# Kernel optimization log

Measured on AMD Instinct MI355X. Metric: run time of the kernel, lower is better.

The kernel has to match this reference:

```python
import jax, jax.numpy as jnp
import numpy as np

GROUPS = 32
EPS = 1e-5
NUM_HEADS = 8

def group_norm(x, w, b):
    # x: [B, C, H, W], normalize over (C//G, H, W) per group
    B, C, H, W = x.shape
    xg = x.reshape(B, GROUPS, C // GROUPS, H, W)
    mean = xg.mean(axis=(2, 3, 4), keepdims=True)
    var = xg.var(axis=(2, 3, 4), keepdims=True)
    xg = (xg - mean) * jax.lax.rsqrt(var + EPS)
    x = xg.reshape(B, C, H, W)
    return x * w[None, :, None, None] + b[None, :, None, None]

def setup_inputs() -> dict:
    key = jax.random.key(0)
    ks = jax.random.split(key, 3)
    C = 512
    x = jax.random.normal(ks[0], (8, C, 32, 32), dtype=jnp.float32)
    gn_w = jnp.ones((C,), jnp.float32)
    gn_b = jnp.zeros((C,), jnp.float32)
    # 1x1 conv weights stored as [out, in] matrices
    qkv_w = jax.random.normal(ks[1], (3 * C, C), dtype=jnp.float32) * (C ** -0.5)
    qkv_b = jnp.zeros((3 * C,), jnp.float32)
    proj_w = jax.random.normal(ks[2], (C, C), dtype=jnp.float32) * (C ** -0.5)
    proj_b = jnp.zeros((C,), jnp.float32)
    return {"x": x, "gn_w": gn_w, "gn_b": gn_b, "qkv_w": qkv_w,
            "qkv_b": qkv_b, "proj_w": proj_w, "proj_b": proj_b}

def reference(x, gn_w, gn_b, qkv_w, qkv_b, proj_w, proj_b):
    B, C, H, W = x.shape
    nh = NUM_HEADS
    hd = C // nh
    N = H * W
    residual = x
    xn = group_norm(x, gn_w, gn_b)
    # 1x1 conv == channel matmul: [B, 3C, H, W]
    qkv = jnp.einsum('bchw,oc->bohw', xn, qkv_w) + qkv_b[None, :, None, None]
    # [B, 3, nh, hd, N] -> q/k/v each [B, nh, N, hd]
    qkv = qkv.reshape(B, 3, nh, hd, N).transpose(1, 0, 2, 4, 3)
    q, k, v = qkv[0], qkv[1], qkv[2]
    scale = hd ** -0.5
    attn = jnp.einsum('bhqd,bhkd->bhqk', q, k) * scale
    attn = jax.nn.softmax(attn, axis=-1)
    out = jnp.einsum('bhqk,bhkd->bhqd', attn, v)  # [B, nh, N, hd]
    out = out.transpose(0, 1, 3, 2).reshape(B, C, H, W)
    out = jnp.einsum('bchw,oc->bohw', out, proj_w) + proj_b[None, :, None, None]
    return out + residual
```

## Files before the change

kernel.cpp:

```cpp
#include <hip/hip_runtime.h>


typedef __bf16 bf16;
typedef __bf16 bf16x8 __attribute__((ext_vector_type(8)));
typedef __bf16 bf16x4 __attribute__((ext_vector_type(4)));
typedef float  f32x4  __attribute__((ext_vector_type(4)));

#define MFMA_16x16x32(A, B, C) __builtin_amdgcn_mfma_f32_16x16x32_bf16((A), (B), (C), 0, 0, 0)

static __device__ __forceinline__ void async_stage_128x32(
    const bf16* __restrict__ g0, bf16* lds, int tid) {
  const int wv = tid >> 6, ln = tid & 63;
#pragma unroll
  for (int cc = 0; cc < 2; ++cc) {
    const int c = wv + cc * 4;
    const bf16* g = g0 + (size_t)(c * 16 + (ln >> 2)) * 512 + (ln & 3) * 8;
    __builtin_amdgcn_global_load_lds(
        (const __attribute__((address_space(1))) void*)g,
        (__attribute__((address_space(3))) void*)(lds + c * 512),
        16, 0, 0);
  }
}

static __device__ __forceinline__ void async_stage_64x32(
    const bf16* __restrict__ g0, bf16* lds, int tid) {
  const int wv = tid >> 6, ln = tid & 63;
  const bf16* g = g0 + (size_t)(wv * 16 + (ln >> 2)) * 512 + (ln & 3) * 8;
  __builtin_amdgcn_global_load_lds(
      (const __attribute__((address_space(1))) void*)g,
      (__attribute__((address_space(3))) void*)(lds + wv * 512),
      16, 0, 0);
}

__global__ __launch_bounds__(256) void gn_fused_kernel(
    const float* __restrict__ x,
    const float* __restrict__ gn_w, const float* __restrict__ gn_b,
    const float* __restrict__ qw, const float* __restrict__ pw,
    bf16* __restrict__ wq, bf16* __restrict__ wp, bf16* __restrict__ xn_t) {
  const int t = threadIdx.x;
  if (blockIdx.x >= 256) {
    const int idx = (blockIdx.x - 256) * 256 + t;
    if (idx < 196608) {
      float4 v = ((const float4*)qw)[idx];
      bf16x4 o = { (bf16)v.x, (bf16)v.y, (bf16)v.z, (bf16)v.w };
      *(bf16x4*)(&wq[idx * 4]) = o;
    }
    if (idx < 65536) {
      float4 v = ((const float4*)pw)[idx];
      bf16x4 o = { (bf16)v.x, (bf16)v.y, (bf16)v.z, (bf16)v.w };
      *(bf16x4*)(&wp[idx * 4]) = o;
    }
    return;
  }
  const int bg = blockIdx.x;
  const int b = bg >> 5, g = bg & 31;
  const int c0 = g * 16;
  const float4* p = (const float4*)(x + ((size_t)b * 512 + c0) * 1024);
  float4 v[16];
  float s = 0.f, s2 = 0.f;
#pragma unroll
  for (int i = 0; i < 16; ++i) {
    v[i] = p[t + 256 * i];
    s  += (v[i].x + v[i].y) + (v[i].z + v[i].w);
    s2 += (v[i].x * v[i].x + v[i].y * v[i].y) + (v[i].z * v[i].z + v[i].w * v[i].w);
  }
#pragma unroll
  for (int d = 1; d < 64; d <<= 1) {
    s  += __shfl_xor(s,  d);
    s2 += __shfl_xor(s2, d);
  }
  __shared__ float as[4], as2[4];
  __shared__ float scs[16], shs[16];
  if ((t & 63) == 0) { as[t >> 6] = s; as2[t >> 6] = s2; }
  __syncthreads();
  if (t < 16) {
    float S  = as[0] + as[1] + as[2] + as[3];
    float S2 = as2[0] + as2[1] + as2[2] + as2[3];
    float m  = S * (1.0f / 16384.0f);
    float rs = rsqrtf(S2 * (1.0f / 16384.0f) - m * m + 1e-5f);
    float sc = rs * gn_w[c0 + t];
    scs[t] = sc;
    shs[t] = gn_b[c0 + t] - m * sc;
  }
  __syncthreads();
  bf16* ob = xn_t + ((size_t)b * 1024 + 4 * t) * 512 + c0;
#pragma unroll
  for (int j = 0; j < 4; ++j) {
    bf16 tmp[16];
#pragma unroll
    for (int i = 0; i < 16; ++i) {
      float val = (j == 0) ? v[i].x : (j == 1) ? v[i].y : (j == 2) ? v[i].z : v[i].w;
      tmp[i] = (bf16)(val * scs[i] + shs[i]);
    }
    *(bf16x8*)(ob + (size_t)j * 512)     = *(bf16x8*)(tmp);
    *(bf16x8*)(ob + (size_t)j * 512 + 8) = *(bf16x8*)(tmp + 8);
  }
}

__global__ __launch_bounds__(256) void qkv_gemm_kernel(
    const bf16* __restrict__ W, const bf16* __restrict__ xn_t,
    const float* __restrict__ qkv_b, bf16* __restrict__ qkv_t,
    bf16* __restrict__ v_t) {
  const int n0 = blockIdx.x * 128;
  const int o0 = blockIdx.y * 128;
  const int b  = blockIdx.z;
  __shared__ bf16 As[2][128 * 32];
  __shared__ bf16 Bs[2][128 * 32];
  const int tid = threadIdx.x, ln = tid & 63, wv = tid >> 6;
  const int mw = (wv >> 1) * 64, nw = (wv & 1) * 64;
  const int l15 = ln & 15, lg = ln >> 4;
  const bool isV = (o0 >= 1024);
  const bf16* gA = W + (size_t)o0 * 512;
  const bf16* gB = xn_t + ((size_t)b * 1024 + n0) * 512;
  f32x4 acc[4][4] = {};
  async_stage_128x32(gA, As[0], tid);
  async_stage_128x32(gB, Bs[0], tid);
  for (int it = 0; it < 16; ++it) {
    __syncthreads();
    const int cur = it & 1, nxt = cur ^ 1;
    if (it < 15) {
      async_stage_128x32(gA + (it + 1) * 32, As[nxt], tid);
      async_stage_128x32(gB + (it + 1) * 32, Bs[nxt], tid);
    }
    bf16x8 af[4], bfr[4];
#pragma unroll
    for (int mi = 0; mi < 4; ++mi)
      af[mi] = *(const bf16x8*)(&As[cur][(mw + mi * 16 + l15) * 32 + lg * 8]);
#pragma unroll
    for (int nj = 0; nj < 4; ++nj)
      bfr[nj] = *(const bf16x8*)(&Bs[cur][(nw + nj * 16 + l15) * 32 + lg * 8]);
    if (!isV) {
#pragma unroll
      for (int mi = 0; mi < 4; ++mi)
#pragma unroll
        for (int nj = 0; nj < 4; ++nj)
          acc[mi][nj] = MFMA_16x16x32(af[mi], bfr[nj], acc[mi][nj]);
    } else {
#pragma unroll
      for (int mi = 0; mi < 4; ++mi)
#pragma unroll
        for (int nj = 0; nj < 4; ++nj)
          acc[mi][nj] = MFMA_16x16x32(bfr[nj], af[mi], acc[mi][nj]);
    }
  }
  if (!isV) {
    const float qs = (o0 < 512) ? 0.125f * 1.44269504089f : 1.0f;
#pragma unroll
    for (int mi = 0; mi < 4; ++mi) {
      const int o = o0 + mw + mi * 16 + lg * 4;
      const float b0 = qkv_b[o], b1 = qkv_b[o + 1], b2 = qkv_b[o + 2], b3 = qkv_b[o + 3];
#pragma unroll
      for (int nj = 0; nj < 4; ++nj) {
        const int n = n0 + nw + nj * 16 + l15;
        f32x4 v = acc[mi][nj];
        bf16x4 st = { (bf16)((v.x + b0) * qs), (bf16)((v.y + b1) * qs),
                      (bf16)((v.z + b2) * qs), (bf16)((v.w + b3) * qs) };
        *(bf16x4*)(&qkv_t[((size_t)b * 1024 + n) * 1536 + o]) = st;
      }
    }
  } else {
#pragma unroll
    for (int mi = 0; mi < 4; ++mi) {
      const int o  = o0 + mw + mi * 16 + l15;
      const int hd = o - 1024;
      const float bias = qkv_b[o];
#pragma unroll
      for (int nj = 0; nj < 4; ++nj) {
        const int n = n0 + nw + nj * 16 + lg * 4;
        f32x4 v = acc[mi][nj];
        bf16x4 st = { (bf16)(v.x + bias), (bf16)(v.y + bias),
                      (bf16)(v.z + bias), (bf16)(v.w + bias) };
        *(bf16x4*)(&v_t[((size_t)b * 512 + hd) * 1024 + n]) = st;
      }
    }
  }
}

__global__ __launch_bounds__(512, 4) void attn_kernel(
    const bf16* __restrict__ qkv_t, const bf16* __restrict__ v_t,
    bf16* __restrict__ at_t) {
  const int qt = blockIdx.y;
  const int b  = blockIdx.x >> 3;
  const int h  = blockIdx.x & 7;
  __shared__ __align__(16) char smem[73728];
  const int tid = threadIdx.x, ln = tid & 63, wv = tid >> 6;
  const int half = wv >> 2, w4 = wv & 3;
  const int l15 = ln & 15, g = ln >> 4;
  bf16* Kt = (bf16*)(smem + half * 18432);
  bf16* Vt = Kt + 64 * 72;
  bf16* Pme = (bf16*)(smem + 36864) + wv * 32 * 72;
  const bf16* hq  = qkv_t + (size_t)b * 1024 * 1536 + h * 64;
  const bf16* hk  = hq + 512;
  const bf16* vtb = v_t + (size_t)(b * 8 + h) * 64 * 1024;

  const int qb = qt * 128 + w4 * 32;
  bf16x8 qf[2][2];
#pragma unroll
  for (int m = 0; m < 2; ++m)
#pragma unroll
    for (int ks = 0; ks < 2; ++ks)
      qf[m][ks] = *(const bf16x8*)(hq + (size_t)(qb + m * 16 + l15) * 1536 + ks * 32 + g * 8);

  f32x4 oacc[2][4] = {};
  float lst[2] = { 0.f, 0.f };

  const int t256 = tid & 255;
  const int srow = t256 >> 2, scg = (t256 & 3) * 16;
  const int kt0 = half * 8;
  bf16x8 kpre0 = *(const bf16x8*)(hk + (size_t)(kt0 * 64 + srow) * 1536 + scg);
  bf16x8 kpre1 = *(const bf16x8*)(hk + (size_t)(kt0 * 64 + srow) * 1536 + scg + 8);
  bf16x8 vpre0 = *(const bf16x8*)(vtb + (size_t)srow * 1024 + kt0 * 64 + scg);
  bf16x8 vpre1 = *(const bf16x8*)(vtb + (size_t)srow * 1024 + kt0 * 64 + scg + 8);

  for (int i = 0; i < 8; ++i) {
    __syncthreads();
    *(bf16x8*)(&Kt[srow * 72 + scg])     = kpre0;
    *(bf16x8*)(&Kt[srow * 72 + scg + 8]) = kpre1;
    *(bf16x8*)(&Vt[srow * 72 + scg])     = vpre0;
    *(bf16x8*)(&Vt[srow * 72 + scg + 8]) = vpre1;
    __syncthreads();
    if (i < 7) {
      const int ktn = kt0 + i + 1;
      const bf16* hk2  = hk  + (size_t)(ktn * 64 + srow) * 1536 + scg;
      const bf16* vtb2 = vtb + (size_t)srow * 1024 + ktn * 64 + scg;
      kpre0 = *(const bf16x8*)(hk2);
      kpre1 = *(const bf16x8*)(hk2 + 8);
      vpre0 = *(const bf16x8*)(vtb2);
      vpre1 = *(const bf16x8*)(vtb2 + 8);
    }

    bf16x8 kf[4][2];
#pragma unroll
    for (int kj = 0; kj < 4; ++kj)
#pragma unroll
      for (int ks = 0; ks < 2; ++ks)
        kf[kj][ks] = *(const bf16x8*)(&Kt[(kj * 16 + l15) * 72 + ks * 32 + g * 8]);

#pragma unroll
    for (int m = 0; m < 2; ++m) {
      f32x4 st[4] = {};
#pragma unroll
      for (int ks = 0; ks < 2; ++ks)
#pragma unroll
        for (int kj = 0; kj < 4; ++kj)
          st[kj] = MFMA_16x16x32(kf[kj][ks], qf[m][ks], st[kj]);
      float rs = 0.f;
#pragma unroll
      for (int kj = 0; kj < 4; ++kj) {
        float e0 = exp2f(st[kj][0]);
        float e1 = exp2f(st[kj][1]);
        float e2 = exp2f(st[kj][2]);
        float e3 = exp2f(st[kj][3]);
        rs += (e0 + e1) + (e2 + e3);
        bf16x4 pe = { (bf16)e0, (bf16)e1, (bf16)e2, (bf16)e3 };
        *(bf16x4*)(&Pme[(m * 16 + l15) * 72 + kj * 16 + g * 4]) = pe;
      }
      lst[m] += rs;
    }

#pragma unroll
    for (int ks = 0; ks < 2; ++ks) {
      bf16x8 vf[4];
#pragma unroll
      for (int dt = 0; dt < 4; ++dt)
        vf[dt] = *(const bf16x8*)(&Vt[(dt * 16 + l15) * 72 + ks * 32 + g * 8]);
#pragma unroll
      for (int m = 0; m < 2; ++m) {
        bf16x8 pf = *(const bf16x8*)(&Pme[(m * 16 + l15) * 72 + ks * 32 + g * 8]);
#pragma unroll
        for (int dt = 0; dt < 4; ++dt)
          oacc[m][dt] = MFMA_16x16x32(vf[dt], pf, oacc[m][dt]);
      }
    }
  }

  float lfull[2];
#pragma unroll
  for (int m = 0; m < 2; ++m) {
    float l = lst[m];
    l += __shfl_xor(l, 16);
    l += __shfl_xor(l, 32);
    lfull[m] = l;
  }

  float* MB  = (float*)smem;
  float* MLb = (float*)(smem + 36864);
  __syncthreads();
  if (half == 1) {
    float* mb = MB + w4 * (32 * 68);
#pragma unroll
    for (int m = 0; m < 2; ++m) {
#pragma unroll
      for (int dt = 0; dt < 4; ++dt)
        *(f32x4*)(mb + (m * 16 + l15) * 68 + dt * 16 + g * 4) = oacc[m][dt];
      if (g == 0) MLb[w4 * 32 + (m * 16 + l15)] = lfull[m];
    }
  }
  __syncthreads();
  if (half == 0) {
    const float* mb = MB + w4 * (32 * 68);
#pragma unroll
    for (int m = 0; m < 2; ++m) {
      const float lB  = MLb[w4 * 32 + (m * 16 + l15)];
      const float inv = 1.0f / (lfull[m] + lB);
      const int q = qb + m * 16 + l15;
#pragma unroll
      for (int dt = 0; dt < 4; ++dt) {
        f32x4 ob = *(const f32x4*)(mb + (m * 16 + l15) * 68 + dt * 16 + g * 4);
        bf16x4 ov = { (bf16)((oacc[m][dt][0] + ob[0]) * inv),
                      (bf16)((oacc[m][dt][1] + ob[1]) * inv),
                      (bf16)((oacc[m][dt][2] + ob[2]) * inv),
                      (bf16)((oacc[m][dt][3] + ob[3]) * inv) };
        *(bf16x4*)(&at_t[((size_t)b * 1024 + q) * 512 + h * 64 + dt * 16 + g * 4]) = ov;
      }
    }
  }
}

__global__ __launch_bounds__(256) void proj_gemm_kernel(
    const bf16* __restrict__ at_t, const bf16* __restrict__ wp,
    const float* __restrict__ proj_b, const float* __restrict__ x,
    float* __restrict__ out) {
  const int i0 = blockIdx.x * 64;
  const int c0 = blockIdx.y * 128;
  const int b  = blockIdx.z;
  __shared__ bf16 As[2][64 * 32];
  __shared__ bf16 Bs[2][128 * 32];
  const int tid = threadIdx.x, ln = tid & 63, wv = tid >> 6;
  const int mw = (wv >> 1) * 32, nw = (wv & 1) * 64;
  const int l15 = ln & 15, lg = ln >> 4;
  const bf16* gA = at_t + ((size_t)b * 1024 + i0) * 512;
  const bf16* gB = wp + (size_t)c0 * 512;
  f32x4 acc[2][4] = {};
  async_stage_64x32(gA, As[0], tid);
  async_stage_128x32(gB, Bs[0], tid);
  for (int it = 0; it < 16; ++it) {
    __syncthreads();
    const int cur = it & 1, nxt = cur ^ 1;
    if (it < 15) {
      async_stage_64x32(gA + (it + 1) * 32, As[nxt], tid);
      async_stage_128x32(gB + (it + 1) * 32, Bs[nxt], tid);
    }
    bf16x8 af[2], bfr[4];
#pragma unroll
    for (int mi = 0; mi < 2; ++mi)
      af[mi] = *(const bf16x8*)(&As[cur][(mw + mi * 16 + l15) * 32 + lg * 8]);
#pragma unroll
    for (int nj = 0; nj < 4; ++nj)
      bfr[nj] = *(const bf16x8*)(&Bs[cur][(nw + nj * 16 + l15) * 32 + lg * 8]);
#pragma unroll
    for (int mi = 0; mi < 2; ++mi)
#pragma unroll
      for (int nj = 0; nj < 4; ++nj)
        acc[mi][nj] = MFMA_16x16x32(af[mi], bfr[nj], acc[mi][nj]);
  }
#pragma unroll
  for (int mi = 0; mi < 2; ++mi) {
    const int i = i0 + mw + mi * 16 + lg * 4;
#pragma unroll
    for (int nj = 0; nj < 4; ++nj) {
      const int c = c0 + nw + nj * 16 + l15;
      const float bias = proj_b[c];
      const size_t off = ((size_t)b * 512 + c) * 1024 + i;
      const float4 res = *(const float4*)(x + off);
      f32x4 v = acc[mi][nj];
      float4 ov;
      ov.x = v.x + bias + res.x;
      ov.y = v.y + bias + res.y;
      ov.z = v.z + bias + res.z;
      ov.w = v.w + bias + res.w;
      *(float4*)(out + off) = ov;
    }
  }
}

extern "C" void kernel_launch(void* const* d_in, const int* in_sizes, int n_in,
                              void* d_out, int out_size, void* d_ws, size_t ws_size,
                              hipStream_t stream) {
  (void)in_sizes; (void)n_in; (void)out_size; (void)ws_size;
  const float* x      = (const float*)d_in[0];
  const float* gn_w   = (const float*)d_in[1];
  const float* gn_b   = (const float*)d_in[2];
  const float* qkv_w  = (const float*)d_in[3];
  const float* qkv_b  = (const float*)d_in[4];
  const float* proj_w = (const float*)d_in[5];
  const float* proj_b = (const float*)d_in[6];
  float* out = (float*)d_out;

  char* ws = (char*)d_ws;
  bf16* wq    = (bf16*)ws;
  bf16* wp    = wq + (size_t)1536 * 512;
  bf16* xn_t  = wp + (size_t)512 * 512;
  bf16* qkv_t = xn_t + (size_t)8 * 1024 * 512;
  bf16* at_t  = qkv_t + (size_t)8 * 1024 * 1536;
  bf16* v_t   = at_t + (size_t)8 * 1024 * 512;

  hipLaunchKernelGGL(gn_fused_kernel, dim3(1280),     dim3(256), 0, stream,
                     x, gn_w, gn_b, qkv_w, proj_w, wq, wp, xn_t);
  hipLaunchKernelGGL(qkv_gemm_kernel, dim3(8, 12, 8), dim3(256), 0, stream,
                     wq, xn_t, qkv_b, qkv_t, v_t);
  hipLaunchKernelGGL(attn_kernel,     dim3(64, 8),    dim3(512), 0, stream,
                     qkv_t, v_t, at_t);
  hipLaunchKernelGGL(proj_gemm_kernel,dim3(16, 4, 8), dim3(256), 0, stream,
                     at_t, wp, proj_b, x, out);
}
```

Before: 158.3 us.

## Rework attention inner loop with 32x32 MFMA, register-resident P, double-buffered K/V

```diff
diff --git a/kernel.cpp b/kernel.cpp
--- a/kernel.cpp
+++ b/kernel.cpp
@@ -5,8 +5,17 @@
 typedef __bf16 bf16x8 __attribute__((ext_vector_type(8)));
 typedef __bf16 bf16x4 __attribute__((ext_vector_type(4)));
 typedef float  f32x4  __attribute__((ext_vector_type(4)));
+typedef float  f32x16 __attribute__((ext_vector_type(16)));
+typedef unsigned u32x4 __attribute__((ext_vector_type(4)));
 
 #define MFMA_16x16x32(A, B, C) __builtin_amdgcn_mfma_f32_16x16x32_bf16((A), (B), (C), 0, 0, 0)
+#define MFMA_32x32x16(A, B, C) __builtin_amdgcn_mfma_f32_32x32x16_bf16((A), (B), (C), 0, 0, 0)
+
+static __device__ __forceinline__ unsigned cvt_pk_bf16(float a, float b) {
+  unsigned r;
+  asm("v_cvt_pk_bf16_f32 %0, %1, %2" : "=v"(r) : "v"(a), "v"(b));
+  return r;
+}
 
 static __device__ __forceinline__ void async_stage_128x32(
     const bf16* __restrict__ g0, bf16* lds, int tid) {
@@ -185,135 +194,128 @@
   __shared__ __align__(16) char smem[73728];
   const int tid = threadIdx.x, ln = tid & 63, wv = tid >> 6;
   const int half = wv >> 2, w4 = wv & 3;
-  const int l15 = ln & 15, g = ln >> 4;
-  bf16* Kt = (bf16*)(smem + half * 18432);
-  bf16* Vt = Kt + 64 * 72;
-  bf16* Pme = (bf16*)(smem + 36864) + wv * 32 * 72;
+  const int l31 = ln & 31, hi = ln >> 5;
   const bf16* hq  = qkv_t + (size_t)b * 1024 * 1536 + h * 64;
   const bf16* hk  = hq + 512;
   const bf16* vtb = v_t + (size_t)(b * 8 + h) * 64 * 1024;
 
   const int qb = qt * 128 + w4 * 32;
-  bf16x8 qf[2][2];
-#pragma unroll
-  for (int m = 0; m < 2; ++m)
-#pragma unroll
-    for (int ks = 0; ks < 2; ++ks)
-      qf[m][ks] = *(const bf16x8*)(hq + (size_t)(qb + m * 16 + l15) * 1536 + ks * 32 + g * 8);
-
-  f32x4 oacc[2][4] = {};
-  float lst[2] = { 0.f, 0.f };
+  bf16x8 qf[4];
+#pragma unroll
+  for (int ks = 0; ks < 4; ++ks)
+    qf[ks] = *(const bf16x8*)(hq + (size_t)(qb + l31) * 1536 + ks * 16 + hi * 8);
+
+  f32x16 oacc[2] = {};
+  float lst = 0.f;
 
   const int t256 = tid & 255;
   const int srow = t256 >> 2, scg = (t256 & 3) * 16;
   const int kt0 = half * 8;
-  bf16x8 kpre0 = *(const bf16x8*)(hk + (size_t)(kt0 * 64 + srow) * 1536 + scg);
-  bf16x8 kpre1 = *(const bf16x8*)(hk + (size_t)(kt0 * 64 + srow) * 1536 + scg + 8);
-  bf16x8 vpre0 = *(const bf16x8*)(vtb + (size_t)srow * 1024 + kt0 * 64 + scg);
-  bf16x8 vpre1 = *(const bf16x8*)(vtb + (size_t)srow * 1024 + kt0 * 64 + scg + 8);
+
+  bf16x8 s0, s1, s2, s3;
+  {
+    const bf16* gk = hk  + (size_t)(kt0 * 64 + srow) * 1536 + scg;
+    const bf16* gv = vtb + (size_t)srow * 1024 + kt0 * 64 + scg;
+    s0 = *(const bf16x8*)(gk);
+    s1 = *(const bf16x8*)(gk + 8);
+    s2 = *(const bf16x8*)(gv);
+    s3 = *(const bf16x8*)(gv + 8);
+    bf16* Kt = (bf16*)(smem + half * 18432);
+    bf16* Vt = Kt + 64 * 72;
+    *(bf16x8*)(&Kt[srow * 72 + scg])     = s0;
+    *(bf16x8*)(&Kt[srow * 72 + scg + 8]) = s1;
+    *(bf16x8*)(&Vt[srow * 72 + scg])     = s2;
+    *(bf16x8*)(&Vt[srow * 72 + scg + 8]) = s3;
+  }
 
   for (int i = 0; i < 8; ++i) {
     __syncthreads();
-    *(bf16x8*)(&Kt[srow * 72 + scg])     = kpre0;
-    *(bf16x8*)(&Kt[srow * 72 + scg + 8]) = kpre1;
-    *(bf16x8*)(&Vt[srow * 72 + scg])     = vpre0;
-    *(bf16x8*)(&Vt[srow * 72 + scg + 8]) = vpre1;
-    __syncthreads();
     if (i < 7) {
-      const int ktn = kt0 + i + 1;
-      const bf16* hk2  = hk  + (size_t)(ktn * 64 + srow) * 1536 + scg;
-      const bf16* vtb2 = vtb + (size_t)srow * 1024 + ktn * 64 + scg;
-      kpre0 = *(const bf16x8*)(hk2);
-      kpre1 = *(const bf16x8*)(hk2 + 8);
-      vpre0 = *(const bf16x8*)(vtb2);
-      vpre1 = *(const bf16x8*)(vtb2 + 8);
-    }
-
-    bf16x8 kf[4][2];
-#pragma unroll
-    for (int kj = 0; kj < 4; ++kj)
-#pragma unroll
-      for (int ks = 0; ks < 2; ++ks)
-        kf[kj][ks] = *(const bf16x8*)(&Kt[(kj * 16 + l15) * 72 + ks * 32 + g * 8]);
-
-#pragma unroll
-    for (int m = 0; m < 2; ++m) {
-      f32x4 st[4] = {};
-#pragma unroll
-      for (int ks = 0; ks < 2; ++ks)
-#pragma unroll
-        for (int kj = 0; kj < 4; ++kj)
-          st[kj] = MFMA_16x16x32(kf[kj][ks], qf[m][ks], st[kj]);
-      float rs = 0.f;
-#pragma unroll
-      for (int kj = 0; kj < 4; ++kj) {
-        float e0 = exp2f(st[kj][0]);
-        float e1 = exp2f(st[kj][1]);
-        float e2 = exp2f(st[kj][2]);
-        float e3 = exp2f(st[kj][3]);
-        rs += (e0 + e1) + (e2 + e3);
-        bf16x4 pe = { (bf16)e0, (bf16)e1, (bf16)e2, (bf16)e3 };
-        *(bf16x4*)(&Pme[(m * 16 + l15) * 72 + kj * 16 + g * 4]) = pe;
-      }
-      lst[m] += rs;
-    }
-
-#pragma unroll
-    for (int ks = 0; ks < 2; ++ks) {
-      bf16x8 vf[4];
-#pragma unroll
-      for (int dt = 0; dt < 4; ++dt)
-        vf[dt] = *(const bf16x8*)(&Vt[(dt * 16 + l15) * 72 + ks * 32 + g * 8]);
-#pragma unroll
-      for (int m = 0; m < 2; ++m) {
-        bf16x8 pf = *(const bf16x8*)(&Pme[(m * 16 + l15) * 72 + ks * 32 + g * 8]);
-#pragma unroll
-        for (int dt = 0; dt < 4; ++dt)
-          oacc[m][dt] = MFMA_16x16x32(vf[dt], pf, oacc[m][dt]);
-      }
-    }
-  }
-
-  float lfull[2];
-#pragma unroll
-  for (int m = 0; m < 2; ++m) {
-    float l = lst[m];
-    l += __shfl_xor(l, 16);
-    l += __shfl_xor(l, 32);
-    lfull[m] = l;
-  }
+      const int kt = kt0 + i + 1;
+      const bf16* gk = hk  + (size_t)(kt * 64 + srow) * 1536 + scg;
+      const bf16* gv = vtb + (size_t)srow * 1024 + kt * 64 + scg;
+      s0 = *(const bf16x8*)(gk);
+      s1 = *(const bf16x8*)(gk + 8);
+      s2 = *(const bf16x8*)(gv);
+      s3 = *(const bf16x8*)(gv + 8);
+    }
+    const bf16* Kt = (const bf16*)(smem + (i & 1) * 36864 + half * 18432);
+    const bf16* Vt = Kt + 64 * 72;
+
+#pragma unroll
+    for (int kk = 0; kk < 2; ++kk) {
+      const int kvb = kk * 32;
+      f32x16 st = {};
+#pragma unroll
+      for (int ks = 0; ks < 4; ++ks) {
+        bf16x8 kf = *(const bf16x8*)(&Kt[(kvb + l31) * 72 + ks * 16 + hi * 8]);
+        st = MFMA_32x32x16(kf, qf[ks], st);
+      }
+#pragma unroll
+      for (int r = 0; r < 16; ++r) st[r] = exp2f(st[r]);
+      lst += ((st[0] + st[1]) + (st[2] + st[3])) + ((st[4] + st[5]) + (st[6] + st[7]))
+           + ((st[8] + st[9]) + (st[10] + st[11])) + ((st[12] + st[13]) + (st[14] + st[15]));
+#pragma unroll
+      for (int t = 0; t < 2; ++t) {
+        unsigned x0 = cvt_pk_bf16(st[t * 8 + 0], st[t * 8 + 1]);
+        unsigned x1 = cvt_pk_bf16(st[t * 8 + 2], st[t * 8 + 3]);
+        unsigned y0 = cvt_pk_bf16(st[t * 8 + 4], st[t * 8 + 5]);
+        unsigned y1 = cvt_pk_bf16(st[t * 8 + 6], st[t * 8 + 7]);
+        asm("v_permlane32_swap_b32 %0, %1" : "+v"(x0), "+v"(y0));
+        asm("v_permlane32_swap_b32 %0, %1" : "+v"(x1), "+v"(y1));
+        u32x4 pu = { x0, x1, y0, y1 };
+        bf16x8 pb = __builtin_bit_cast(bf16x8, pu);
+#pragma unroll
+        for (int dt = 0; dt < 2; ++dt) {
+          bf16x8 vf = *(const bf16x8*)(&Vt[(dt * 32 + l31) * 72 + kvb + t * 16 + hi * 8]);
+          oacc[dt] = MFMA_32x32x16(vf, pb, oacc[dt]);
+        }
+      }
+    }
+
+    if (i < 7) {
+      bf16* Ktn = (bf16*)(smem + ((i + 1) & 1) * 36864 + half * 18432);
+      bf16* Vtn = Ktn + 64 * 72;
+      *(bf16x8*)(&Ktn[srow * 72 + scg])     = s0;
+      *(bf16x8*)(&Ktn[srow * 72 + scg + 8]) = s1;
+      *(bf16x8*)(&Vtn[srow * 72 + scg])     = s2;
+      *(bf16x8*)(&Vtn[srow * 72 + scg + 8]) = s3;
+    }
+  }
+
+  const float lf = lst + __shfl_xor(lst, 32);
 
   float* MB  = (float*)smem;
-  float* MLb = (float*)(smem + 36864);
+  float* MLb = (float*)(smem + 34816);
   __syncthreads();
   if (half == 1) {
     float* mb = MB + w4 * (32 * 68);
 #pragma unroll
-    for (int m = 0; m < 2; ++m) {
-#pragma unroll
-      for (int dt = 0; dt < 4; ++dt)
-        *(f32x4*)(mb + (m * 16 + l15) * 68 + dt * 16 + g * 4) = oacc[m][dt];
-      if (g == 0) MLb[w4 * 32 + (m * 16 + l15)] = lfull[m];
-    }
+    for (int dt = 0; dt < 2; ++dt)
+#pragma unroll
+      for (int rr = 0; rr < 4; ++rr) {
+        f32x4 v = { oacc[dt][rr * 4 + 0], oacc[dt][rr * 4 + 1],
+                    oacc[dt][rr * 4 + 2], oacc[dt][rr * 4 + 3] };
+        *(f32x4*)(mb + l31 * 68 + dt * 32 + rr * 8 + hi * 4) = v;
+      }
+    if (hi == 0) MLb[w4 * 32 + l31] = lf;
   }
   __syncthreads();
   if (half == 0) {
     const float* mb = MB + w4 * (32 * 68);
-#pragma unroll
-    for (int m = 0; m < 2; ++m) {
-      const float lB  = MLb[w4 * 32 + (m * 16 + l15)];
-      const float inv = 1.0f / (lfull[m] + lB);
-      const int q = qb + m * 16 + l15;
-#pragma unroll
-      for (int dt = 0; dt < 4; ++dt) {
-        f32x4 ob = *(const f32x4*)(mb + (m * 16 + l15) * 68 + dt * 16 + g * 4);
-        bf16x4 ov = { (bf16)((oacc[m][dt][0] + ob[0]) * inv),
-                      (bf16)((oacc[m][dt][1] + ob[1]) * inv),
-                      (bf16)((oacc[m][dt][2] + ob[2]) * inv),
-                      (bf16)((oacc[m][dt][3] + ob[3]) * inv) };
-        *(bf16x4*)(&at_t[((size_t)b * 1024 + q) * 512 + h * 64 + dt * 16 + g * 4]) = ov;
-      }
-    }
+    const float inv = 1.0f / (lf + MLb[w4 * 32 + l31]);
+    const int q = qb + l31;
+#pragma unroll
+    for (int dt = 0; dt < 2; ++dt)
+#pragma unroll
+      for (int rr = 0; rr < 4; ++rr) {
+        f32x4 ob = *(const f32x4*)(mb + l31 * 68 + dt * 32 + rr * 8 + hi * 4);
+        bf16x4 ov = { (bf16)((oacc[dt][rr * 4 + 0] + ob[0]) * inv),
+                      (bf16)((oacc[dt][rr * 4 + 1] + ob[1]) * inv),
+                      (bf16)((oacc[dt][rr * 4 + 2] + ob[2]) * inv),
+                      (bf16)((oacc[dt][rr * 4 + 3] + ob[3]) * inv) };
+        *(bf16x4*)(&at_t[((size_t)b * 1024 + q) * 512 + h * 64 + dt * 32 + rr * 8 + hi * 4]) = ov;
+      }
   }
 }
 
```

New measurement: 154.2 us. 1.03x faster.
